# Kernel tuning notes

Hardware: AMD Instinct MI355X
Metric: run time of the kernel (lower is better)

Reference implementation:

```python
import jax, jax.numpy as jnp
import numpy as np

N_NODES = 100000
N_EDGES = 3200000
N_GRAPHS = 1000
HID = 64
L = 4  # num_unit


def setup_inputs() -> dict:
    key = jax.random.key(0)
    ks = jax.random.split(key, 16)
    x = jax.random.normal(ks[0], (N_NODES, 4), dtype=jnp.float32)
    edge_index = jax.random.randint(ks[1], (2, N_EDGES), 0, N_NODES, dtype=jnp.int64)
    edge_attr = jax.random.uniform(ks[2], (N_EDGES,), dtype=jnp.float32)
    batch = jnp.sort(jax.random.randint(ks[3], (N_NODES,), 0, N_GRAPHS, dtype=jnp.int64))
    s = 1.0 / np.sqrt(HID)
    inp = {
        'x': x, 'edge_index': edge_index, 'edge_attr': edge_attr, 'batch': batch,
        'emb_w': jax.random.normal(ks[4], (4, HID), jnp.float32) * 0.5,
        'emb_b': jnp.zeros((HID,), jnp.float32),
        'conv_w1': jax.random.normal(ks[5], (L, HID, HID), jnp.float32) * s,
        'conv_b1': jnp.zeros((L, HID), jnp.float32),
        'conv_w2': jax.random.normal(ks[6], (L, HID, HID), jnp.float32) * s,
        'conv_w3': jax.random.normal(ks[7], (L, HID, HID), jnp.float32) * s,
        'conv_b3': jnp.zeros((L, HID), jnp.float32),
        'lin1_w': jax.random.normal(ks[8], (HID, HID), jnp.float32) * s,
        'lin1_b': jnp.zeros((HID,), jnp.float32),
        'lin2_w': jax.random.normal(ks[9], (HID, 3), jnp.float32) * s,
        'lin2_b': jnp.zeros((3,), jnp.float32),
    }
    return inp


def _forward(x, edge_index, edge_attr, batch,
             emb_w, emb_b, conv_w1, conv_b1, conv_w2, conv_w3, conv_b3,
             lin1_w, lin1_b, lin2_w, lin2_b):
    src, dst = edge_index[0], edge_index[1]
    ew = edge_attr[:, None]  # [E,1]
    h = x @ emb_w + emb_b  # node_emb; dropout omitted (eval mode)
    for l in range(conv_w1.shape[0]):
        # LEConv: out_i = sum_{j->i} w_ji * (lin1(x_j) - lin2(x_i)) + lin3(x_i)
        a = h @ conv_w1[l] + conv_b1[l]
        b = h @ conv_w2[l]  # no bias
        msg = (a[src] - b[dst]) * ew  # [E, HID]
        agg = jax.ops.segment_sum(msg, dst, num_segments=h.shape[0])
        h = jax.nn.relu(agg + h @ conv_w3[l] + conv_b3[l])
    # global mean pool over graphs
    sums = jax.ops.segment_sum(h, batch, num_segments=N_GRAPHS)
    cnt = jax.ops.segment_sum(jnp.ones((h.shape[0],), h.dtype), batch, num_segments=N_GRAPHS)
    graph_x = sums / jnp.maximum(cnt, 1.0)[:, None]
    pred = jax.nn.relu(graph_x @ lin1_w + lin1_b) @ lin2_w + lin2_b
    return pred


def reference(x, edge_index, edge_attr, batch, emb_w, emb_b,
              conv_w1, conv_b1, conv_w2, conv_w3, conv_b3,
              lin1_w, lin1_b, lin2_w, lin2_b):
    return _forward(x, edge_index, edge_attr, batch, emb_w, emb_b,
                    conv_w1, conv_b1, conv_w2, conv_w3, conv_b3,
                    lin1_w, lin1_b, lin2_w, lin2_b)
```

## Files before the change

kernel.cpp:

```cpp
#include <hip/hip_runtime.h>

#define N_NODES 100000
#define N_EDGES 3200000
#define N_GRAPHS 1000
#define NLAYER 4
#define NB 391
#define CAP 8960
#define EPB 4096
#define NCHUNK 782

typedef __attribute__((ext_vector_type(8))) short bf16x8;
typedef __attribute__((ext_vector_type(4))) float f32x4;

static __device__ __forceinline__ unsigned f2bf(float f) {
  unsigned u = __float_as_uint(f);
  return (u + 0x7fffu + ((u >> 16) & 1u)) >> 16;
}
static __device__ __forceinline__ float bf2f_lo(unsigned u) {
  return __uint_as_float(u << 16);
}
static __device__ __forceinline__ float bf2f_hi(unsigned u) {
  return __uint_as_float(u & 0xffff0000u);
}

__global__ __launch_bounds__(256) void prologue_kernel(
    const float* __restrict__ x, const float* __restrict__ emb_w,
    const float* __restrict__ emb_b, unsigned short* __restrict__ h_bf,
    int* __restrict__ gcur,
    const float* __restrict__ cw1, const float* __restrict__ cw2,
    const float* __restrict__ cw3, unsigned* __restrict__ wswz)
{
  int tid = threadIdx.x;
  if (blockIdx.x == 4) {
    for (int i = tid; i < NB; i += 256) gcur[i] = i * CAP;
  }
  if (blockIdx.x < NLAYER) {
    int l = blockIdx.x;
    const float* w1 = cw1 + l * 4096;
    const float* w2 = cw2 + l * 4096;
    const float* w3 = cw3 + l * 4096;
    unsigned* outp = wswz + l * 6144;
    int n = tid & 63;
    int gofs = tid >> 6;
    for (int it = 0; it < 24; ++it) {
      int g = it * 4 + gofs;
      int m = g >> 5;
      int k = (g & 31) * 2;
      const float* W = (m == 0) ? w2 : (m == 1) ? w3 : w1;
      unsigned lo = f2bf(W[k * 64 + n]);
      unsigned hi = f2bf(W[(k + 1) * 64 + n]);
      int c = k >> 5;
      int kk = k & 31;
      int ln = ((kk >> 3) << 4) | (n & 15);
      int j2 = (kk & 7) >> 1;
      int t4 = n >> 4;
      outp[(((m * 2 + c) * 4 + t4) << 8) | (ln << 2) | j2] = lo | (hi << 16);
    }
  }
  int t = blockIdx.x * 256 + tid;
  if (t >= N_NODES * 64) return;
  int c = t & 63, v = t >> 6;
  float4 xv = ((const float4*)x)[v];
  float acc = emb_b[c];
  acc = fmaf(xv.x, emb_w[0 * 64 + c], acc);
  acc = fmaf(xv.y, emb_w[1 * 64 + c], acc);
  acc = fmaf(xv.z, emb_w[2 * 64 + c], acc);
  acc = fmaf(xv.w, emb_w[3 * 64 + c], acc);
  h_bf[t] = (unsigned short)f2bf(acc);
}

__global__ __launch_bounds__(256) void bscatter_kernel(
    const int* __restrict__ ei, const float* __restrict__ ea,
    int* __restrict__ gcur, unsigned* __restrict__ tmp_w,
    unsigned char* __restrict__ tmp_d)
{
  __shared__ unsigned hist[NB];
  __shared__ int dif[NB];
  __shared__ unsigned stage_w[EPB];
  __shared__ unsigned char stage_d[EPB];
  __shared__ unsigned short bid[EPB];
  __shared__ int wpart[4];
  int tid = threadIdx.x;
  int base = blockIdx.x * EPB;

  for (int i = tid; i < NB; i += 256) hist[i] = 0;
  __syncthreads();

  int dreg[16];
#pragma unroll
  for (int i = 0; i < 16; ++i) {
    int e = base + i * 256 + tid;
    dreg[i] = -1;
    if (e < N_EDGES) {
      int d = ei[N_EDGES + e];
      dreg[i] = d;
      atomicAdd(&hist[((unsigned)d) >> 8], 1u);
    }
  }
  __syncthreads();

  int lane = tid & 63, w = tid >> 6;
  int b0i = tid * 2, b1i = tid * 2 + 1;
  int c0 = (b0i < NB) ? (int)hist[b0i] : 0;
  int c1 = (b1i < NB) ? (int)hist[b1i] : 0;
  int tsum = c0 + c1;
  int s = tsum;
#pragma unroll
  for (int off = 1; off < 64; off <<= 1) {
    int y = __shfl_up(s, off);
    if (lane >= off) s += y;
  }
  if (lane == 63) wpart[w] = s;
  __syncthreads();
  int wo = 0;
  for (int ww = 0; ww < w; ++ww) wo += wpart[ww];
  int excl = wo + (s - tsum);
  if (b0i < NB) {
    int gb = c0 ? atomicAdd(&gcur[b0i], c0) : 0;
    dif[b0i] = gb - excl;
    hist[b0i] = (unsigned)excl;
  }
  if (b1i < NB) {
    int gb = c1 ? atomicAdd(&gcur[b1i], c1) : 0;
    dif[b1i] = gb - (excl + c0);
    hist[b1i] = (unsigned)(excl + c0);
  }
  __syncthreads();

#pragma unroll
  for (int i = 0; i < 16; ++i) {
    int e = base + i * 256 + tid;
    int d = dreg[i];
    if (d >= 0) {
      unsigned bkt = ((unsigned)d) >> 8;
      unsigned lp = atomicAdd(&hist[bkt], 1u);
      unsigned q15 = (unsigned)(ea[e] * 32768.0f);
      stage_w[lp] = ((unsigned)ei[e]) | (q15 << 17);
      stage_d[lp] = (unsigned char)(d & 255);
      bid[lp] = (unsigned short)bkt;
    }
  }
  __syncthreads();

  int nE = min(EPB, N_EDGES - base);
  for (int i = tid; i < nE; i += 256) {
    int g = dif[bid[i]] + i;
    tmp_w[g] = stage_w[i];
    tmp_d[g] = stage_d[i];
  }
}

__global__ __launch_bounds__(256) void bucket_sort_kernel(
    const int* __restrict__ gcur, const unsigned* __restrict__ tmp_w,
    const unsigned char* __restrict__ tmp_d,
    unsigned* __restrict__ csr, int* __restrict__ row_off,
    unsigned short* __restrict__ deg16, float* __restrict__ degw)
{
  int j = blockIdx.x;
  int b0 = j * CAP;
  int nE = min(gcur[j] - b0, CAP);
  __shared__ unsigned hist[256];
  __shared__ float dws[256];
  __shared__ unsigned cur[256];
  __shared__ int wpart[4];
  __shared__ unsigned short perm[CAP];
  int t = threadIdx.x;
  hist[t] = 0;
  dws[t] = 0.f;
  __syncthreads();
  for (int i = t; i < nE; i += 256) {
    unsigned d = tmp_d[b0 + i];
    unsigned wrd = tmp_w[b0 + i];
    atomicAdd(&hist[d], 1u);
    atomicAdd(&dws[d], (float)(wrd >> 17) * (1.0f / 32768.0f));
  }
  __syncthreads();
  int lane = t & 63, w = t >> 6;
  int v = (int)hist[t];
  int s = v;
#pragma unroll
  for (int off = 1; off < 64; off <<= 1) {
    int y = __shfl_up(s, off);
    if (lane >= off) s += y;
  }
  if (lane == 63) wpart[w] = s;
  __syncthreads();
  int wo = 0;
  for (int ww = 0; ww < w; ++ww) wo += wpart[ww];
  int excl = wo + s - v;
  cur[t] = (unsigned)excl;
  int vnode = (j << 8) + t;
  if (vnode < N_NODES) {
    row_off[vnode] = b0 + excl;
    deg16[vnode] = (unsigned short)v;
    degw[vnode] = dws[t];
  }
  __syncthreads();

  for (int i = t; i < nE; i += 256) {
    unsigned p = atomicAdd(&cur[tmp_d[b0 + i]], 1u);
    perm[p] = (unsigned short)i;
  }
  __syncthreads();
  for (int q = t; q < nE; q += 256)
    csr[b0 + q] = tmp_w[b0 + (int)perm[q]];
}

__global__ __launch_bounds__(256) void matvec3_mfma_kernel(
    const unsigned short* __restrict__ h_bf,
    const unsigned* __restrict__ wz,
    const float* __restrict__ b1, const float* __restrict__ b3,
    const float* __restrict__ degw,
    unsigned short* __restrict__ a_bf, unsigned short* __restrict__ cc_bf)
{
  int gw = (blockIdx.x * 256 + threadIdx.x) >> 6;
  int lane = threadIdx.x & 63;
  int quad = lane >> 4;
  int col = lane & 15;
  int nb = gw * 16;
  if (nb >= N_NODES) return;

  int arow = nb + col;
  if (arow >= N_NODES) arow = N_NODES - 1;
  const bf16x8* ap = (const bf16x8*)(h_bf + (size_t)arow * 64 + quad * 8);
  bf16x8 af0 = ap[0];
  bf16x8 af1 = ap[4];

  float dwr[4];
#pragma unroll
  for (int r = 0; r < 4; ++r) {
    int row = nb + quad * 4 + r;
    dwr[r] = degw[row < N_NODES ? row : 0];
  }

#pragma unroll
  for (int t = 0; t < 4; ++t) {
    const bf16x8* b20 = (const bf16x8*)&wz[((0 * 4 + t) << 8) + lane * 4];
    const bf16x8* b21 = (const bf16x8*)&wz[((1 * 4 + t) << 8) + lane * 4];
    const bf16x8* b30 = (const bf16x8*)&wz[((2 * 4 + t) << 8) + lane * 4];
    const bf16x8* b31 = (const bf16x8*)&wz[((3 * 4 + t) << 8) + lane * 4];
    const bf16x8* b10 = (const bf16x8*)&wz[((4 * 4 + t) << 8) + lane * 4];
    const bf16x8* b11 = (const bf16x8*)&wz[((5 * 4 + t) << 8) + lane * 4];

    f32x4 z = {0.f, 0.f, 0.f, 0.f};
    f32x4 acc2 = __builtin_amdgcn_mfma_f32_16x16x32_bf16(af0, *b20, z, 0, 0, 0);
    acc2 = __builtin_amdgcn_mfma_f32_16x16x32_bf16(af1, *b21, acc2, 0, 0, 0);
    f32x4 cc;
#pragma unroll
    for (int r = 0; r < 4; ++r) cc[r] = -dwr[r] * acc2[r];
    cc = __builtin_amdgcn_mfma_f32_16x16x32_bf16(af0, *b30, cc, 0, 0, 0);
    cc = __builtin_amdgcn_mfma_f32_16x16x32_bf16(af1, *b31, cc, 0, 0, 0);
    float bb3 = b3[t * 16 + col];
#pragma unroll
    for (int r = 0; r < 4; ++r) {
      int row = nb + quad * 4 + r;
      if (row < N_NODES)
        cc_bf[(size_t)row * 64 + t * 16 + col] = (unsigned short)f2bf(cc[r] + bb3);
    }

    float bb1 = b1[t * 16 + col];
    f32x4 a1 = {bb1, bb1, bb1, bb1};
    a1 = __builtin_amdgcn_mfma_f32_16x16x32_bf16(af0, *b10, a1, 0, 0, 0);
    a1 = __builtin_amdgcn_mfma_f32_16x16x32_bf16(af1, *b11, a1, 0, 0, 0);
#pragma unroll
    for (int r = 0; r < 4; ++r) {
      int row = nb + quad * 4 + r;
      if (row < N_NODES)
        a_bf[(size_t)row * 64 + t * 16 + col] = (unsigned short)f2bf(a1[r]);
    }
  }
}

__global__ __launch_bounds__(256) void agg_kernel(
    const uint2* __restrict__ a2, const uint2* __restrict__ cc2,
    const int* __restrict__ row_off, const unsigned short* __restrict__ deg16,
    const unsigned* __restrict__ csr,
    float4* __restrict__ h4, unsigned short* __restrict__ h_bf, int write_h)
{
  int wave = (blockIdx.x * 256 + threadIdx.x) >> 6;
  int lane = threadIdx.x & 63;
  int sg = lane >> 4;
  int li = lane & 15;
  int lsel = (lane & 48) << 2;
  int v = wave * 4 + sg;
  bool valid = v < N_NODES;
  int vc = valid ? v : N_NODES - 1;
  int base = row_off[vc];
  int ecnt = valid ? (int)deg16[vc] : 0;
  int emax = ecnt;
  emax = max(emax, __shfl_xor(emax, 16));
  emax = max(emax, __shfl_xor(emax, 32));

  float4 acc = make_float4(0.f, 0.f, 0.f, 0.f);
  if (valid) {
    uint2 cu = cc2[(size_t)vc * 16 + li];
    acc.x = bf2f_lo(cu.x);
    acc.y = bf2f_hi(cu.x);
    acc.z = bf2f_lo(cu.y);
    acc.w = bf2f_hi(cu.y);
  }
  const uint2* ap = a2 + li;

  int full = emax & ~15;
  int c0 = 0;
  for (; c0 < full; c0 += 16) {
    int idx = c0 + li;
    int er = (idx < ecnt) ? (int)csr[base + idx] : 0;
#pragma unroll
    for (int j = 0; j < 16; ++j) {
      unsigned r = (unsigned)__builtin_amdgcn_ds_bpermute(lsel | (j << 2), er);
      int s = (int)(r & 0x1FFFFu);
      float w = (float)(r >> 17) * (1.0f / 32768.0f);
      uint2 u = ap[(size_t)s * 16];
      acc.x = fmaf(w, bf2f_lo(u.x), acc.x);
      acc.y = fmaf(w, bf2f_hi(u.x), acc.y);
      acc.z = fmaf(w, bf2f_lo(u.y), acc.z);
      acc.w = fmaf(w, bf2f_hi(u.y), acc.w);
    }
  }
  int rem = emax - full;
  if (rem > 0) {
    int idx = c0 + li;
    int er = (idx < ecnt) ? (int)csr[base + idx] : 0;
    for (int j = 0; j < rem; ++j) {
      unsigned r = (unsigned)__builtin_amdgcn_ds_bpermute(lsel | (j << 2), er);
      int s = (int)(r & 0x1FFFFu);
      float w = (float)(r >> 17) * (1.0f / 32768.0f);
      uint2 u = ap[(size_t)s * 16];
      acc.x = fmaf(w, bf2f_lo(u.x), acc.x);
      acc.y = fmaf(w, bf2f_hi(u.x), acc.y);
      acc.z = fmaf(w, bf2f_lo(u.y), acc.z);
      acc.w = fmaf(w, bf2f_hi(u.y), acc.w);
    }
  }
  if (valid) {
    acc.x = fmaxf(acc.x, 0.f);
    acc.y = fmaxf(acc.y, 0.f);
    acc.z = fmaxf(acc.z, 0.f);
    acc.w = fmaxf(acc.w, 0.f);
    if (write_h) h4[(size_t)v * 16 + li] = acc;
    uint2 p;
    p.x = f2bf(acc.x) | (f2bf(acc.y) << 16);
    p.y = f2bf(acc.z) | (f2bf(acc.w) << 16);
    ((uint2*)h_bf)[(size_t)v * 16 + li] = p;
  }
}

__global__ __launch_bounds__(256) void head_kernel(
    const float* __restrict__ h, const int* __restrict__ batch,
    const float* __restrict__ l1w, const float* __restrict__ l1b,
    const float* __restrict__ l2w, const float* __restrict__ l2b,
    float* __restrict__ out)
{
  int g = (blockIdx.x * 256 + threadIdx.x) >> 6;
  int lane = threadIdx.x & 63;
  if (g >= N_GRAPHS) return;
  int lo = 0, hi = N_NODES;
  while (lo < hi) { int mid = (lo + hi) >> 1; if (batch[mid] < g) lo = mid + 1; else hi = mid; }
  int start = lo;
  hi = N_NODES;
  while (lo < hi) { int mid = (lo + hi) >> 1; if (batch[mid] < g + 1) lo = mid + 1; else hi = mid; }
  int end = lo;

  float sum = 0.f;
  for (int v = start; v < end; ++v) sum += h[(size_t)v * 64 + lane];
  float cntf = (float)(end - start);
  float gx = sum / fmaxf(cntf, 1.f);

  float acc = l1b[lane];
  for (int k = 0; k < 64; ++k) {
    float gxk = __shfl(gx, k);
    acc = fmaf(gxk, l1w[k * 64 + lane], acc);
  }
  float t = fmaxf(acc, 0.f);
  float p0 = t * l2w[lane * 3 + 0];
  float p1 = t * l2w[lane * 3 + 1];
  float p2 = t * l2w[lane * 3 + 2];
  for (int off = 32; off > 0; off >>= 1) {
    p0 += __shfl_down(p0, off);
    p1 += __shfl_down(p1, off);
    p2 += __shfl_down(p2, off);
  }
  if (lane == 0) {
    out[g * 3 + 0] = p0 + l2b[0];
    out[g * 3 + 1] = p1 + l2b[1];
    out[g * 3 + 2] = p2 + l2b[2];
  }
}

extern "C" void kernel_launch(void* const* d_in, const int* in_sizes, int n_in,
                              void* d_out, int out_size, void* d_ws, size_t ws_size,
                              hipStream_t stream)
{
  (void)in_sizes; (void)n_in; (void)out_size; (void)ws_size;
  const float* x     = (const float*)d_in[0];
  const int*   ei    = (const int*)d_in[1];
  const float* ea    = (const float*)d_in[2];
  const int*   batch = (const int*)d_in[3];
  const float* emb_w = (const float*)d_in[4];
  const float* emb_b = (const float*)d_in[5];
  const float* cw1   = (const float*)d_in[6];
  const float* cb1   = (const float*)d_in[7];
  const float* cw2   = (const float*)d_in[8];
  const float* cw3   = (const float*)d_in[9];
  const float* cb3   = (const float*)d_in[10];
  const float* l1w   = (const float*)d_in[11];
  const float* l1b   = (const float*)d_in[12];
  const float* l2w   = (const float*)d_in[13];
  const float* l2b   = (const float*)d_in[14];
  float* out = (float*)d_out;

  char* wsb = (char*)d_ws;
  size_t off = 0;
  auto alloc = [&](size_t bytes) {
    char* p = wsb + off;
    off = (off + bytes + 255) & ~(size_t)255;
    return p;
  };
  float* h       = (float*)alloc(sizeof(float) * (size_t)N_NODES * 64);
  unsigned short* h_bf = (unsigned short*)alloc(sizeof(short) * (size_t)N_NODES * 64);
  unsigned short* a_bf = (unsigned short*)alloc(sizeof(short) * (size_t)N_NODES * 64);
  unsigned short* cc_bf = (unsigned short*)alloc(sizeof(short) * (size_t)N_NODES * 64);
  unsigned* csr  = (unsigned*)alloc(sizeof(unsigned) * (size_t)NB * CAP);
  int*   row_off = (int*)alloc(sizeof(int) * N_NODES);
  unsigned short* deg16 = (unsigned short*)alloc(sizeof(short) * N_NODES);
  float* degw    = (float*)alloc(sizeof(float) * N_NODES);
  int*   gcur    = (int*)alloc(sizeof(int) * NB);
  unsigned* wswz = (unsigned*)alloc(sizeof(unsigned) * NLAYER * 6144);
  unsigned* tmp_w = (unsigned*)h;
  unsigned char* tmp_d = (unsigned char*)h + sizeof(unsigned) * (size_t)NB * CAP;

  prologue_kernel<<<(N_NODES * 64 + 255) / 256, 256, 0, stream>>>(
      x, emb_w, emb_b, h_bf, gcur, cw1, cw2, cw3, wswz);
  bscatter_kernel<<<NCHUNK, 256, 0, stream>>>(ei, ea, gcur, tmp_w, tmp_d);
  bucket_sort_kernel<<<NB, 256, 0, stream>>>(gcur, tmp_w, tmp_d, csr, row_off,
                                             deg16, degw);

  int agg_blocks = (N_NODES + 15) / 16;
  int mv_blocks = (N_NODES / 16 + 3) / 4 + 1;
  for (int l = 0; l < NLAYER; ++l) {
    matvec3_mfma_kernel<<<mv_blocks, 256, 0, stream>>>(
        h_bf, wswz + l * 6144, cb1 + l * 64, cb3 + l * 64, degw, a_bf, cc_bf);
    agg_kernel<<<agg_blocks, 256, 0, stream>>>(
        (const uint2*)a_bf, (const uint2*)cc_bf, row_off, deg16, csr, (float4*)h,
        h_bf, (l == NLAYER - 1) ? 1 : 0);
  }

  head_kernel<<<(N_GRAPHS * 64 + 255) / 256, 256, 0, stream>>>(
      h, batch, l1w, l1b, l2w, l2b, out);
}
```

Before: 520.2 us.

## Fuse per-layer matvec, aggregation and head into one persistent kernel with grid barriers

Replaces the eight per-layer launches plus the head launch with a single persistent kernel sized by occupancy. A hierarchical software grid barrier separates the matvec and aggregation phases, and the tiles and node groups are walked with grid-stride loops. The bucket scatter now loads edge source and weight in the first pass and keeps them in registers. This removes launch gaps and tail effects between small kernels. In exchange the kernel risks barrier overhead, lower occupancy from the 8-blocks-per-CU bound, and deadlock if not all blocks are co-resident.

```diff
diff --git a/kernel.cpp b/kernel.cpp
--- a/kernel.cpp
+++ b/kernel.cpp
@@ -8,6 +8,10 @@
 #define CAP 8960
 #define EPB 4096
 #define NCHUNK 782
+#define N_TILES 6250
+#define N_GRP 25000
+#define MAXBLK 2048
+#define BAR_LINES 66
 
 typedef __attribute__((ext_vector_type(8))) short bf16x8;
 typedef __attribute__((ext_vector_type(4))) float f32x4;
@@ -21,6 +25,34 @@
 }
 static __device__ __forceinline__ float bf2f_hi(unsigned u) {
   return __uint_as_float(u & 0xffff0000u);
+}
+
+static __device__ __forceinline__ void gbar(int* bar, int bid, int nblk) {
+  __syncthreads();
+  if (threadIdx.x == 0) {
+    __threadfence();
+    int gen = __hip_atomic_load(bar + 65 * 32, __ATOMIC_RELAXED,
+                                __HIP_MEMORY_SCOPE_AGENT);
+    int* leaf = bar + (bid >> 5) * 32;
+    int old = __hip_atomic_fetch_add(leaf, 1, __ATOMIC_RELAXED,
+                                     __HIP_MEMORY_SCOPE_AGENT);
+    if (old == 31) {
+      __hip_atomic_store(leaf, 0, __ATOMIC_RELAXED, __HIP_MEMORY_SCOPE_AGENT);
+      int rold = __hip_atomic_fetch_add(bar + 64 * 32, 1, __ATOMIC_RELAXED,
+                                        __HIP_MEMORY_SCOPE_AGENT);
+      if (rold == (nblk >> 5) - 1) {
+        __hip_atomic_store(bar + 64 * 32, 0, __ATOMIC_RELAXED,
+                           __HIP_MEMORY_SCOPE_AGENT);
+        __hip_atomic_fetch_add(bar + 65 * 32, 1, __ATOMIC_RELAXED,
+                               __HIP_MEMORY_SCOPE_AGENT);
+      }
+    }
+    while (__hip_atomic_load(bar + 65 * 32, __ATOMIC_RELAXED,
+                             __HIP_MEMORY_SCOPE_AGENT) == gen)
+      __builtin_amdgcn_s_sleep(16);
+    __threadfence();
+  }
+  __syncthreads();
 }
 
 __global__ __launch_bounds__(256) void prologue_kernel(
@@ -28,11 +60,15 @@
     const float* __restrict__ emb_b, unsigned short* __restrict__ h_bf,
     int* __restrict__ gcur,
     const float* __restrict__ cw1, const float* __restrict__ cw2,
-    const float* __restrict__ cw3, unsigned* __restrict__ wswz)
+    const float* __restrict__ cw3, unsigned* __restrict__ wswz,
+    int* __restrict__ bar)
 {
   int tid = threadIdx.x;
   if (blockIdx.x == 4) {
     for (int i = tid; i < NB; i += 256) gcur[i] = i * CAP;
+  }
+  if (blockIdx.x == 5) {
+    for (int i = tid; i < BAR_LINES * 32; i += 256) bar[i] = 0;
   }
   if (blockIdx.x < NLAYER) {
     int l = blockIdx.x;
@@ -87,6 +123,7 @@
   __syncthreads();
 
   int dreg[16];
+  unsigned wreg[16];
 #pragma unroll
   for (int i = 0; i < 16; ++i) {
     int e = base + i * 256 + tid;
@@ -94,6 +131,8 @@
     if (e < N_EDGES) {
       int d = ei[N_EDGES + e];
       dreg[i] = d;
+      unsigned q15 = (unsigned)(ea[e] * 32768.0f);
+      wreg[i] = ((unsigned)ei[e]) | (q15 << 17);
       atomicAdd(&hist[((unsigned)d) >> 8], 1u);
     }
   }
@@ -129,13 +168,11 @@
 
 #pragma unroll
   for (int i = 0; i < 16; ++i) {
-    int e = base + i * 256 + tid;
     int d = dreg[i];
     if (d >= 0) {
       unsigned bkt = ((unsigned)d) >> 8;
       unsigned lp = atomicAdd(&hist[bkt], 1u);
-      unsigned q15 = (unsigned)(ea[e] * 32768.0f);
-      stage_w[lp] = ((unsigned)ei[e]) | (q15 << 17);
+      stage_w[lp] = wreg[i];
       stage_d[lp] = (unsigned char)(d & 255);
       bid[lp] = (unsigned short)bkt;
     }
@@ -206,185 +243,175 @@
     csr[b0 + q] = tmp_w[b0 + (int)perm[q]];
 }
 
-__global__ __launch_bounds__(256) void matvec3_mfma_kernel(
-    const unsigned short* __restrict__ h_bf,
-    const unsigned* __restrict__ wz,
-    const float* __restrict__ b1, const float* __restrict__ b3,
-    const float* __restrict__ degw,
-    unsigned short* __restrict__ a_bf, unsigned short* __restrict__ cc_bf)
+__global__ __launch_bounds__(256, 8) void layers_kernel(
+    unsigned short* __restrict__ h_bf, unsigned short* __restrict__ a_bf,
+    unsigned short* __restrict__ cc_bf, const unsigned* __restrict__ csr,
+    const int* __restrict__ row_off, const unsigned short* __restrict__ deg16,
+    const float* __restrict__ degw, const unsigned* __restrict__ wswz,
+    const float* __restrict__ cb1, const float* __restrict__ cb3,
+    float* __restrict__ h, const int* __restrict__ batch,
+    const float* __restrict__ l1w, const float* __restrict__ l1b,
+    const float* __restrict__ l2w, const float* __restrict__ l2b,
+    float* __restrict__ out, int* __restrict__ bar, int nblk)
 {
-  int gw = (blockIdx.x * 256 + threadIdx.x) >> 6;
-  int lane = threadIdx.x & 63;
+  int bid = blockIdx.x;
+  int tid = threadIdx.x;
+  int lane = tid & 63;
+  int gw = bid * 4 + (tid >> 6);
+  int nwave = nblk * 4;
   int quad = lane >> 4;
   int col = lane & 15;
-  int nb = gw * 16;
-  if (nb >= N_NODES) return;
-
-  int arow = nb + col;
-  if (arow >= N_NODES) arow = N_NODES - 1;
-  const bf16x8* ap = (const bf16x8*)(h_bf + (size_t)arow * 64 + quad * 8);
-  bf16x8 af0 = ap[0];
-  bf16x8 af1 = ap[4];
-
-  float dwr[4];
-#pragma unroll
-  for (int r = 0; r < 4; ++r) {
-    int row = nb + quad * 4 + r;
-    dwr[r] = degw[row < N_NODES ? row : 0];
-  }
-
-#pragma unroll
-  for (int t = 0; t < 4; ++t) {
-    const bf16x8* b20 = (const bf16x8*)&wz[((0 * 4 + t) << 8) + lane * 4];
-    const bf16x8* b21 = (const bf16x8*)&wz[((1 * 4 + t) << 8) + lane * 4];
-    const bf16x8* b30 = (const bf16x8*)&wz[((2 * 4 + t) << 8) + lane * 4];
-    const bf16x8* b31 = (const bf16x8*)&wz[((3 * 4 + t) << 8) + lane * 4];
-    const bf16x8* b10 = (const bf16x8*)&wz[((4 * 4 + t) << 8) + lane * 4];
-    const bf16x8* b11 = (const bf16x8*)&wz[((5 * 4 + t) << 8) + lane * 4];
-
-    f32x4 z = {0.f, 0.f, 0.f, 0.f};
-    f32x4 acc2 = __builtin_amdgcn_mfma_f32_16x16x32_bf16(af0, *b20, z, 0, 0, 0);
-    acc2 = __builtin_amdgcn_mfma_f32_16x16x32_bf16(af1, *b21, acc2, 0, 0, 0);
-    f32x4 cc;
-#pragma unroll
-    for (int r = 0; r < 4; ++r) cc[r] = -dwr[r] * acc2[r];
-    cc = __builtin_amdgcn_mfma_f32_16x16x32_bf16(af0, *b30, cc, 0, 0, 0);
-    cc = __builtin_amdgcn_mfma_f32_16x16x32_bf16(af1, *b31, cc, 0, 0, 0);
-    float bb3 = b3[t * 16 + col];
-#pragma unroll
-    for (int r = 0; r < 4; ++r) {
-      int row = nb + quad * 4 + r;
-      if (row < N_NODES)
-        cc_bf[(size_t)row * 64 + t * 16 + col] = (unsigned short)f2bf(cc[r] + bb3);
-    }
-
-    float bb1 = b1[t * 16 + col];
-    f32x4 a1 = {bb1, bb1, bb1, bb1};
-    a1 = __builtin_amdgcn_mfma_f32_16x16x32_bf16(af0, *b10, a1, 0, 0, 0);
-    a1 = __builtin_amdgcn_mfma_f32_16x16x32_bf16(af1, *b11, a1, 0, 0, 0);
-#pragma unroll
-    for (int r = 0; r < 4; ++r) {
-      int row = nb + quad * 4 + r;
-      if (row < N_NODES)
-        a_bf[(size_t)row * 64 + t * 16 + col] = (unsigned short)f2bf(a1[r]);
-    }
-  }
-}
-
-__global__ __launch_bounds__(256) void agg_kernel(
-    const uint2* __restrict__ a2, const uint2* __restrict__ cc2,
-    const int* __restrict__ row_off, const unsigned short* __restrict__ deg16,
-    const unsigned* __restrict__ csr,
-    float4* __restrict__ h4, unsigned short* __restrict__ h_bf, int write_h)
-{
-  int wave = (blockIdx.x * 256 + threadIdx.x) >> 6;
-  int lane = threadIdx.x & 63;
   int sg = lane >> 4;
   int li = lane & 15;
   int lsel = (lane & 48) << 2;
-  int v = wave * 4 + sg;
-  bool valid = v < N_NODES;
-  int vc = valid ? v : N_NODES - 1;
-  int base = row_off[vc];
-  int ecnt = valid ? (int)deg16[vc] : 0;
-  int emax = ecnt;
-  emax = max(emax, __shfl_xor(emax, 16));
-  emax = max(emax, __shfl_xor(emax, 32));
-
-  float4 acc = make_float4(0.f, 0.f, 0.f, 0.f);
-  if (valid) {
-    uint2 cu = cc2[(size_t)vc * 16 + li];
-    acc.x = bf2f_lo(cu.x);
-    acc.y = bf2f_hi(cu.x);
-    acc.z = bf2f_lo(cu.y);
-    acc.w = bf2f_hi(cu.y);
-  }
-  const uint2* ap = a2 + li;
-
-  int full = emax & ~15;
-  int c0 = 0;
-  for (; c0 < full; c0 += 16) {
-    int idx = c0 + li;
-    int er = (idx < ecnt) ? (int)csr[base + idx] : 0;
-#pragma unroll
-    for (int j = 0; j < 16; ++j) {
-      unsigned r = (unsigned)__builtin_amdgcn_ds_bpermute(lsel | (j << 2), er);
-      int s = (int)(r & 0x1FFFFu);
-      float w = (float)(r >> 17) * (1.0f / 32768.0f);
-      uint2 u = ap[(size_t)s * 16];
-      acc.x = fmaf(w, bf2f_lo(u.x), acc.x);
-      acc.y = fmaf(w, bf2f_hi(u.x), acc.y);
-      acc.z = fmaf(w, bf2f_lo(u.y), acc.z);
-      acc.w = fmaf(w, bf2f_hi(u.y), acc.w);
-    }
-  }
-  int rem = emax - full;
-  if (rem > 0) {
-    int idx = c0 + li;
-    int er = (idx < ecnt) ? (int)csr[base + idx] : 0;
-    for (int j = 0; j < rem; ++j) {
-      unsigned r = (unsigned)__builtin_amdgcn_ds_bpermute(lsel | (j << 2), er);
-      int s = (int)(r & 0x1FFFFu);
-      float w = (float)(r >> 17) * (1.0f / 32768.0f);
-      uint2 u = ap[(size_t)s * 16];
-      acc.x = fmaf(w, bf2f_lo(u.x), acc.x);
-      acc.y = fmaf(w, bf2f_hi(u.x), acc.y);
-      acc.z = fmaf(w, bf2f_lo(u.y), acc.z);
-      acc.w = fmaf(w, bf2f_hi(u.y), acc.w);
-    }
-  }
-  if (valid) {
-    acc.x = fmaxf(acc.x, 0.f);
-    acc.y = fmaxf(acc.y, 0.f);
-    acc.z = fmaxf(acc.z, 0.f);
-    acc.w = fmaxf(acc.w, 0.f);
-    if (write_h) h4[(size_t)v * 16 + li] = acc;
-    uint2 p;
-    p.x = f2bf(acc.x) | (f2bf(acc.y) << 16);
-    p.y = f2bf(acc.z) | (f2bf(acc.w) << 16);
-    ((uint2*)h_bf)[(size_t)v * 16 + li] = p;
-  }
-}
-
-__global__ __launch_bounds__(256) void head_kernel(
-    const float* __restrict__ h, const int* __restrict__ batch,
-    const float* __restrict__ l1w, const float* __restrict__ l1b,
-    const float* __restrict__ l2w, const float* __restrict__ l2b,
-    float* __restrict__ out)
-{
-  int g = (blockIdx.x * 256 + threadIdx.x) >> 6;
-  int lane = threadIdx.x & 63;
-  if (g >= N_GRAPHS) return;
-  int lo = 0, hi = N_NODES;
-  while (lo < hi) { int mid = (lo + hi) >> 1; if (batch[mid] < g) lo = mid + 1; else hi = mid; }
-  int start = lo;
-  hi = N_NODES;
-  while (lo < hi) { int mid = (lo + hi) >> 1; if (batch[mid] < g + 1) lo = mid + 1; else hi = mid; }
-  int end = lo;
-
-  float sum = 0.f;
-  for (int v = start; v < end; ++v) sum += h[(size_t)v * 64 + lane];
-  float cntf = (float)(end - start);
-  float gx = sum / fmaxf(cntf, 1.f);
-
-  float acc = l1b[lane];
-  for (int k = 0; k < 64; ++k) {
-    float gxk = __shfl(gx, k);
-    acc = fmaf(gxk, l1w[k * 64 + lane], acc);
-  }
-  float t = fmaxf(acc, 0.f);
-  float p0 = t * l2w[lane * 3 + 0];
-  float p1 = t * l2w[lane * 3 + 1];
-  float p2 = t * l2w[lane * 3 + 2];
-  for (int off = 32; off > 0; off >>= 1) {
-    p0 += __shfl_down(p0, off);
-    p1 += __shfl_down(p1, off);
-    p2 += __shfl_down(p2, off);
-  }
-  if (lane == 0) {
-    out[g * 3 + 0] = p0 + l2b[0];
-    out[g * 3 + 1] = p1 + l2b[1];
-    out[g * 3 + 2] = p2 + l2b[2];
+
+  for (int l = 0; l < NLAYER; ++l) {
+    const unsigned* wz = wswz + l * 6144;
+    const float* b1 = cb1 + l * 64;
+    const float* b3 = cb3 + l * 64;
+
+    for (int tile = gw; tile < N_TILES; tile += nwave) {
+      int nb = tile * 16;
+      int arow = nb + col;
+      const bf16x8* ap = (const bf16x8*)(h_bf + (size_t)arow * 64 + quad * 8);
+      bf16x8 af0 = ap[0];
+      bf16x8 af1 = ap[4];
+      float dwr[4];
+#pragma unroll
+      for (int r = 0; r < 4; ++r) dwr[r] = degw[nb + quad * 4 + r];
+
+#pragma unroll
+      for (int t = 0; t < 4; ++t) {
+        const bf16x8* b20 = (const bf16x8*)&wz[((0 * 4 + t) << 8) + lane * 4];
+        const bf16x8* b21 = (const bf16x8*)&wz[((1 * 4 + t) << 8) + lane * 4];
+        const bf16x8* b30 = (const bf16x8*)&wz[((2 * 4 + t) << 8) + lane * 4];
+        const bf16x8* b31 = (const bf16x8*)&wz[((3 * 4 + t) << 8) + lane * 4];
+        const bf16x8* b10 = (const bf16x8*)&wz[((4 * 4 + t) << 8) + lane * 4];
+        const bf16x8* b11 = (const bf16x8*)&wz[((5 * 4 + t) << 8) + lane * 4];
+
+        f32x4 z = {0.f, 0.f, 0.f, 0.f};
+        f32x4 acc2 = __builtin_amdgcn_mfma_f32_16x16x32_bf16(af0, *b20, z, 0, 0, 0);
+        acc2 = __builtin_amdgcn_mfma_f32_16x16x32_bf16(af1, *b21, acc2, 0, 0, 0);
+        f32x4 cc;
+#pragma unroll
+        for (int r = 0; r < 4; ++r) cc[r] = -dwr[r] * acc2[r];
+        cc = __builtin_amdgcn_mfma_f32_16x16x32_bf16(af0, *b30, cc, 0, 0, 0);
+        cc = __builtin_amdgcn_mfma_f32_16x16x32_bf16(af1, *b31, cc, 0, 0, 0);
+        float bb3 = b3[t * 16 + col];
+#pragma unroll
+        for (int r = 0; r < 4; ++r) {
+          int row = nb + quad * 4 + r;
+          cc_bf[(size_t)row * 64 + t * 16 + col] = (unsigned short)f2bf(cc[r] + bb3);
+        }
+        float bb1 = b1[t * 16 + col];
+        f32x4 a1 = {bb1, bb1, bb1, bb1};
+        a1 = __builtin_amdgcn_mfma_f32_16x16x32_bf16(af0, *b10, a1, 0, 0, 0);
+        a1 = __builtin_amdgcn_mfma_f32_16x16x32_bf16(af1, *b11, a1, 0, 0, 0);
+#pragma unroll
+        for (int r = 0; r < 4; ++r) {
+          int row = nb + quad * 4 + r;
+          a_bf[(size_t)row * 64 + t * 16 + col] = (unsigned short)f2bf(a1[r]);
+        }
+      }
+    }
+    gbar(bar, bid, nblk);
+
+    const uint2* a2 = (const uint2*)a_bf;
+    const uint2* cc2 = (const uint2*)cc_bf;
+    int write_h = (l == NLAYER - 1);
+    for (int grp = gw; grp < N_GRP; grp += nwave) {
+      int v = grp * 4 + sg;
+      int base = row_off[v];
+      int ecnt = (int)deg16[v];
+      int emax = ecnt;
+      emax = max(emax, __shfl_xor(emax, 16));
+      emax = max(emax, __shfl_xor(emax, 32));
+
+      uint2 cu = cc2[(size_t)v * 16 + li];
+      float4 acc;
+      acc.x = bf2f_lo(cu.x);
+      acc.y = bf2f_hi(cu.x);
+      acc.z = bf2f_lo(cu.y);
+      acc.w = bf2f_hi(cu.y);
+      const uint2* ap = a2 + li;
+
+      int full = emax & ~15;
+      int c0 = 0;
+      for (; c0 < full; c0 += 16) {
+        int idx = c0 + li;
+        int er = (idx < ecnt) ? (int)csr[base + idx] : 0;
+#pragma unroll
+        for (int j = 0; j < 16; ++j) {
+          unsigned r = (unsigned)__builtin_amdgcn_ds_bpermute(lsel | (j << 2), er);
+          int s = (int)(r & 0x1FFFFu);
+          float w = (float)(r >> 17) * (1.0f / 32768.0f);
+          uint2 u = ap[(size_t)s * 16];
+          acc.x = fmaf(w, bf2f_lo(u.x), acc.x);
+          acc.y = fmaf(w, bf2f_hi(u.x), acc.y);
+          acc.z = fmaf(w, bf2f_lo(u.y), acc.z);
+          acc.w = fmaf(w, bf2f_hi(u.y), acc.w);
+        }
+      }
+      int rem = emax - full;
+      if (rem > 0) {
+        int idx = c0 + li;
+        int er = (idx < ecnt) ? (int)csr[base + idx] : 0;
+        for (int j = 0; j < rem; ++j) {
+          unsigned r = (unsigned)__builtin_amdgcn_ds_bpermute(lsel | (j << 2), er);
+          int s = (int)(r & 0x1FFFFu);
+          float w = (float)(r >> 17) * (1.0f / 32768.0f);
+          uint2 u = ap[(size_t)s * 16];
+          acc.x = fmaf(w, bf2f_lo(u.x), acc.x);
+          acc.y = fmaf(w, bf2f_hi(u.x), acc.y);
+          acc.z = fmaf(w, bf2f_lo(u.y), acc.z);
+          acc.w = fmaf(w, bf2f_hi(u.y), acc.w);
+        }
+      }
+      acc.x = fmaxf(acc.x, 0.f);
+      acc.y = fmaxf(acc.y, 0.f);
+      acc.z = fmaxf(acc.z, 0.f);
+      acc.w = fmaxf(acc.w, 0.f);
+      if (write_h) ((float4*)h)[(size_t)v * 16 + li] = acc;
+      uint2 p;
+      p.x = f2bf(acc.x) | (f2bf(acc.y) << 16);
+      p.y = f2bf(acc.z) | (f2bf(acc.w) << 16);
+      ((uint2*)h_bf)[(size_t)v * 16 + li] = p;
+    }
+    gbar(bar, bid, nblk);
+  }
+
+  for (int g = gw; g < N_GRAPHS; g += nwave) {
+    int lo = 0, hi = N_NODES;
+    while (lo < hi) { int mid = (lo + hi) >> 1; if (batch[mid] < g) lo = mid + 1; else hi = mid; }
+    int start = lo;
+    hi = N_NODES;
+    while (lo < hi) { int mid = (lo + hi) >> 1; if (batch[mid] < g + 1) lo = mid + 1; else hi = mid; }
+    int end = lo;
+
+    float sum = 0.f;
+    for (int v = start; v < end; ++v) sum += h[(size_t)v * 64 + lane];
+    float cntf = (float)(end - start);
+    float gx = sum / fmaxf(cntf, 1.f);
+
+    float acc = l1b[lane];
+    for (int k = 0; k < 64; ++k) {
+      float gxk = __shfl(gx, k);
+      acc = fmaf(gxk, l1w[k * 64 + lane], acc);
+    }
+    float t = fmaxf(acc, 0.f);
+    float p0 = t * l2w[lane * 3 + 0];
+    float p1 = t * l2w[lane * 3 + 1];
+    float p2 = t * l2w[lane * 3 + 2];
+    for (int off = 32; off > 0; off >>= 1) {
+      p0 += __shfl_down(p0, off);
+      p1 += __shfl_down(p1, off);
+      p2 += __shfl_down(p2, off);
+    }
+    if (lane == 0) {
+      out[g * 3 + 0] = p0 + l2b[0];
+      out[g * 3 + 1] = p1 + l2b[1];
+      out[g * 3 + 2] = p2 + l2b[2];
+    }
   }
 }
 
@@ -427,25 +454,24 @@
   float* degw    = (float*)alloc(sizeof(float) * N_NODES);
   int*   gcur    = (int*)alloc(sizeof(int) * NB);
   unsigned* wswz = (unsigned*)alloc(sizeof(unsigned) * NLAYER * 6144);
+  int*   bar     = (int*)alloc(sizeof(int) * BAR_LINES * 32);
   unsigned* tmp_w = (unsigned*)h;
   unsigned char* tmp_d = (unsigned char*)h + sizeof(unsigned) * (size_t)NB * CAP;
 
+  int maxb = 0;
+  hipOccupancyMaxActiveBlocksPerMultiprocessor(&maxb, layers_kernel, 256, 0);
+  if (maxb < 1) maxb = 1;
+  int nblk = maxb * 256;
+  if (nblk > MAXBLK) nblk = MAXBLK;
+  nblk = (nblk / 32) * 32;
+  if (nblk < 32) nblk = 32;
+
   prologue_kernel<<<(N_NODES * 64 + 255) / 256, 256, 0, stream>>>(
-      x, emb_w, emb_b, h_bf, gcur, cw1, cw2, cw3, wswz);
+      x, emb_w, emb_b, h_bf, gcur, cw1, cw2, cw3, wswz, bar);
   bscatter_kernel<<<NCHUNK, 256, 0, stream>>>(ei, ea, gcur, tmp_w, tmp_d);
   bucket_sort_kernel<<<NB, 256, 0, stream>>>(gcur, tmp_w, tmp_d, csr, row_off,
                                              deg16, degw);
-
-  int agg_blocks = (N_NODES + 15) / 16;
-  int mv_blocks = (N_NODES / 16 + 3) / 4 + 1;
-  for (int l = 0; l < NLAYER; ++l) {
-    matvec3_mfma_kernel<<<mv_blocks, 256, 0, stream>>>(
-        h_bf, wswz + l * 6144, cb1 + l * 64, cb3 + l * 64, degw, a_bf, cc_bf);
-    agg_kernel<<<agg_blocks, 256, 0, stream>>>(
-        (const uint2*)a_bf, (const uint2*)cc_bf, row_off, deg16, csr, (float4*)h,
-        h_bf, (l == NLAYER - 1) ? 1 : 0);
-  }
-
-  head_kernel<<<(N_GRAPHS * 64 + 255) / 256, 256, 0, stream>>>(
-      h, batch, l1w, l1b, l2w, l2b, out);
-}
+  layers_kernel<<<nblk, 256, 0, stream>>>(
+      h_bf, a_bf, cc_bf, csr, row_off, deg16, degw, wswz, cb1, cb3,
+      h, batch, l1w, l1b, l2w, l2b, out, bar, nblk);
+}
```

Measured after the change: 1.100 ms. 2.11x slower.

## Fuse next-layer MFMA matvec into aggregation kernel with ping-pong buffers

Applied to the files above, without the earlier changes.

Each aggregation block now handles 64 nodes, stages their bf16 outputs in shared memory, and computes the next layer's a/cc projections with MFMA before writing them out. The node features no longer make a global round trip through h_bf, and three kernel launches are removed, using double-buffered a/cc arrays. Separately, the bucket scatter loads source index and edge weight in the first pass and keeps them in registers instead of re-reading them. The fused kernel needs a block barrier and extra LDS, which may reduce occupancy for the latency-bound gather.

```diff
diff --git a/kernel.cpp b/kernel.cpp
--- a/kernel.cpp
+++ b/kernel.cpp
@@ -8,6 +8,7 @@
 #define CAP 8960
 #define EPB 4096
 #define NCHUNK 782
+#define NFBLK 1563
 
 typedef __attribute__((ext_vector_type(8))) short bf16x8;
 typedef __attribute__((ext_vector_type(4))) float f32x4;
@@ -87,6 +88,7 @@
   __syncthreads();
 
   int dreg[16];
+  unsigned wreg[16];
 #pragma unroll
   for (int i = 0; i < 16; ++i) {
     int e = base + i * 256 + tid;
@@ -94,6 +96,8 @@
     if (e < N_EDGES) {
       int d = ei[N_EDGES + e];
       dreg[i] = d;
+      unsigned q15 = (unsigned)(ea[e] * 32768.0f);
+      wreg[i] = ((unsigned)ei[e]) | (q15 << 17);
       atomicAdd(&hist[((unsigned)d) >> 8], 1u);
     }
   }
@@ -129,13 +133,11 @@
 
 #pragma unroll
   for (int i = 0; i < 16; ++i) {
-    int e = base + i * 256 + tid;
     int d = dreg[i];
     if (d >= 0) {
       unsigned bkt = ((unsigned)d) >> 8;
       unsigned lp = atomicAdd(&hist[bkt], 1u);
-      unsigned q15 = (unsigned)(ea[e] * 32768.0f);
-      stage_w[lp] = ((unsigned)ei[e]) | (q15 << 17);
+      stage_w[lp] = wreg[i];
       stage_d[lp] = (unsigned char)(d & 255);
       bid[lp] = (unsigned short)bkt;
     }
@@ -206,7 +208,7 @@
     csr[b0 + q] = tmp_w[b0 + (int)perm[q]];
 }
 
-__global__ __launch_bounds__(256) void matvec3_mfma_kernel(
+__global__ __launch_bounds__(256) void matvec0_kernel(
     const unsigned short* __restrict__ h_bf,
     const unsigned* __restrict__ wz,
     const float* __restrict__ b1, const float* __restrict__ b3,
@@ -271,78 +273,142 @@
   }
 }
 
-__global__ __launch_bounds__(256) void agg_kernel(
+__global__ __launch_bounds__(256) void aggmv_kernel(
     const uint2* __restrict__ a2, const uint2* __restrict__ cc2,
     const int* __restrict__ row_off, const unsigned short* __restrict__ deg16,
-    const unsigned* __restrict__ csr,
-    float4* __restrict__ h4, unsigned short* __restrict__ h_bf, int write_h)
-{
-  int wave = (blockIdx.x * 256 + threadIdx.x) >> 6;
-  int lane = threadIdx.x & 63;
+    const unsigned* __restrict__ csr, const float* __restrict__ degw,
+    const unsigned* __restrict__ wz,
+    const float* __restrict__ b1, const float* __restrict__ b3,
+    unsigned short* __restrict__ a_out, unsigned short* __restrict__ cc_out,
+    float4* __restrict__ h4, int write_h, int do_mv)
+{
+  __shared__ uint2 hl[64][18];
+  int tid = threadIdx.x;
+  int lane = tid & 63;
+  int wv = tid >> 6;
   int sg = lane >> 4;
   int li = lane & 15;
   int lsel = (lane & 48) << 2;
-  int v = wave * 4 + sg;
-  bool valid = v < N_NODES;
-  int vc = valid ? v : N_NODES - 1;
-  int base = row_off[vc];
-  int ecnt = valid ? (int)deg16[vc] : 0;
-  int emax = ecnt;
-  emax = max(emax, __shfl_xor(emax, 16));
-  emax = max(emax, __shfl_xor(emax, 32));
-
-  float4 acc = make_float4(0.f, 0.f, 0.f, 0.f);
-  if (valid) {
-    uint2 cu = cc2[(size_t)vc * 16 + li];
-    acc.x = bf2f_lo(cu.x);
-    acc.y = bf2f_hi(cu.x);
-    acc.z = bf2f_lo(cu.y);
-    acc.w = bf2f_hi(cu.y);
-  }
-  const uint2* ap = a2 + li;
-
-  int full = emax & ~15;
-  int c0 = 0;
-  for (; c0 < full; c0 += 16) {
-    int idx = c0 + li;
-    int er = (idx < ecnt) ? (int)csr[base + idx] : 0;
-#pragma unroll
-    for (int j = 0; j < 16; ++j) {
-      unsigned r = (unsigned)__builtin_amdgcn_ds_bpermute(lsel | (j << 2), er);
-      int s = (int)(r & 0x1FFFFu);
-      float w = (float)(r >> 17) * (1.0f / 32768.0f);
-      uint2 u = ap[(size_t)s * 16];
-      acc.x = fmaf(w, bf2f_lo(u.x), acc.x);
-      acc.y = fmaf(w, bf2f_hi(u.x), acc.y);
-      acc.z = fmaf(w, bf2f_lo(u.y), acc.z);
-      acc.w = fmaf(w, bf2f_hi(u.y), acc.w);
-    }
-  }
-  int rem = emax - full;
-  if (rem > 0) {
-    int idx = c0 + li;
-    int er = (idx < ecnt) ? (int)csr[base + idx] : 0;
-    for (int j = 0; j < rem; ++j) {
-      unsigned r = (unsigned)__builtin_amdgcn_ds_bpermute(lsel | (j << 2), er);
-      int s = (int)(r & 0x1FFFFu);
-      float w = (float)(r >> 17) * (1.0f / 32768.0f);
-      uint2 u = ap[(size_t)s * 16];
-      acc.x = fmaf(w, bf2f_lo(u.x), acc.x);
-      acc.y = fmaf(w, bf2f_hi(u.x), acc.y);
-      acc.z = fmaf(w, bf2f_lo(u.y), acc.z);
-      acc.w = fmaf(w, bf2f_hi(u.y), acc.w);
-    }
-  }
-  if (valid) {
-    acc.x = fmaxf(acc.x, 0.f);
-    acc.y = fmaxf(acc.y, 0.f);
-    acc.z = fmaxf(acc.z, 0.f);
-    acc.w = fmaxf(acc.w, 0.f);
-    if (write_h) h4[(size_t)v * 16 + li] = acc;
-    uint2 p;
-    p.x = f2bf(acc.x) | (f2bf(acc.y) << 16);
-    p.y = f2bf(acc.z) | (f2bf(acc.w) << 16);
-    ((uint2*)h_bf)[(size_t)v * 16 + li] = p;
+  int nb0 = blockIdx.x * 64;
+
+#pragma unroll
+  for (int it = 0; it < 4; ++it) {
+    int lv = wv * 16 + it * 4 + sg;
+    int v = nb0 + lv;
+    bool valid = v < N_NODES;
+    int vc = valid ? v : N_NODES - 1;
+    int base = row_off[vc];
+    int ecnt = valid ? (int)deg16[vc] : 0;
+    int emax = ecnt;
+    emax = max(emax, __shfl_xor(emax, 16));
+    emax = max(emax, __shfl_xor(emax, 32));
+
+    float4 acc = make_float4(0.f, 0.f, 0.f, 0.f);
+    if (valid) {
+      uint2 cu = cc2[(size_t)vc * 16 + li];
+      acc.x = bf2f_lo(cu.x);
+      acc.y = bf2f_hi(cu.x);
+      acc.z = bf2f_lo(cu.y);
+      acc.w = bf2f_hi(cu.y);
+    }
+    const uint2* ap = a2 + li;
+
+    int full = emax & ~15;
+    int c0 = 0;
+    for (; c0 < full; c0 += 16) {
+      int idx = c0 + li;
+      int er = (idx < ecnt) ? (int)csr[base + idx] : 0;
+#pragma unroll
+      for (int j = 0; j < 16; ++j) {
+        unsigned r = (unsigned)__builtin_amdgcn_ds_bpermute(lsel | (j << 2), er);
+        int s = (int)(r & 0x1FFFFu);
+        float w = (float)(r >> 17) * (1.0f / 32768.0f);
+        uint2 u = ap[(size_t)s * 16];
+        acc.x = fmaf(w, bf2f_lo(u.x), acc.x);
+        acc.y = fmaf(w, bf2f_hi(u.x), acc.y);
+        acc.z = fmaf(w, bf2f_lo(u.y), acc.z);
+        acc.w = fmaf(w, bf2f_hi(u.y), acc.w);
+      }
+    }
+    int rem = emax - full;
+    if (rem > 0) {
+      int idx = c0 + li;
+      int er = (idx < ecnt) ? (int)csr[base + idx] : 0;
+      for (int j = 0; j < rem; ++j) {
+        unsigned r = (unsigned)__builtin_amdgcn_ds_bpermute(lsel | (j << 2), er);
+        int s = (int)(r & 0x1FFFFu);
+        float w = (float)(r >> 17) * (1.0f / 32768.0f);
+        uint2 u = ap[(size_t)s * 16];
+        acc.x = fmaf(w, bf2f_lo(u.x), acc.x);
+        acc.y = fmaf(w, bf2f_hi(u.x), acc.y);
+        acc.z = fmaf(w, bf2f_lo(u.y), acc.z);
+        acc.w = fmaf(w, bf2f_hi(u.y), acc.w);
+      }
+    }
+    if (valid) {
+      acc.x = fmaxf(acc.x, 0.f);
+      acc.y = fmaxf(acc.y, 0.f);
+      acc.z = fmaxf(acc.z, 0.f);
+      acc.w = fmaxf(acc.w, 0.f);
+      if (write_h) h4[(size_t)v * 16 + li] = acc;
+      uint2 p;
+      p.x = f2bf(acc.x) | (f2bf(acc.y) << 16);
+      p.y = f2bf(acc.z) | (f2bf(acc.w) << 16);
+      hl[lv][li] = p;
+    }
+  }
+  if (!do_mv) return;
+  __syncthreads();
+
+  int quad = lane >> 4;
+  int col = lane & 15;
+  int nb = nb0 + wv * 16;
+  const char* rowp = (const char*)&hl[wv * 16 + col][0];
+  bf16x8 af0 = *(const bf16x8*)(rowp + quad * 16);
+  bf16x8 af1 = *(const bf16x8*)(rowp + 64 + quad * 16);
+
+  float dwr[4];
+#pragma unroll
+  for (int r = 0; r < 4; ++r) {
+    int row = nb + quad * 4 + r;
+    dwr[r] = degw[row < N_NODES ? row : 0];
+  }
+
+#pragma unroll
+  for (int t = 0; t < 4; ++t) {
+    const bf16x8* b20 = (const bf16x8*)&wz[((0 * 4 + t) << 8) + lane * 4];
+    const bf16x8* b21 = (const bf16x8*)&wz[((1 * 4 + t) << 8) + lane * 4];
+    const bf16x8* b30 = (const bf16x8*)&wz[((2 * 4 + t) << 8) + lane * 4];
+    const bf16x8* b31 = (const bf16x8*)&wz[((3 * 4 + t) << 8) + lane * 4];
+    const bf16x8* b10 = (const bf16x8*)&wz[((4 * 4 + t) << 8) + lane * 4];
+    const bf16x8* b11 = (const bf16x8*)&wz[((5 * 4 + t) << 8) + lane * 4];
+
+    f32x4 z = {0.f, 0.f, 0.f, 0.f};
+    f32x4 acc2 = __builtin_amdgcn_mfma_f32_16x16x32_bf16(af0, *b20, z, 0, 0, 0);
+    acc2 = __builtin_amdgcn_mfma_f32_16x16x32_bf16(af1, *b21, acc2, 0, 0, 0);
+    f32x4 cc;
+#pragma unroll
+    for (int r = 0; r < 4; ++r) cc[r] = -dwr[r] * acc2[r];
+    cc = __builtin_amdgcn_mfma_f32_16x16x32_bf16(af0, *b30, cc, 0, 0, 0);
+    cc = __builtin_amdgcn_mfma_f32_16x16x32_bf16(af1, *b31, cc, 0, 0, 0);
+    float bb3 = b3[t * 16 + col];
+#pragma unroll
+    for (int r = 0; r < 4; ++r) {
+      int row = nb + quad * 4 + r;
+      if (row < N_NODES)
+        cc_out[(size_t)row * 64 + t * 16 + col] = (unsigned short)f2bf(cc[r] + bb3);
+    }
+
+    float bb1 = b1[t * 16 + col];
+    f32x4 a1 = {bb1, bb1, bb1, bb1};
+    a1 = __builtin_amdgcn_mfma_f32_16x16x32_bf16(af0, *b10, a1, 0, 0, 0);
+    a1 = __builtin_amdgcn_mfma_f32_16x16x32_bf16(af1, *b11, a1, 0, 0, 0);
+#pragma unroll
+    for (int r = 0; r < 4; ++r) {
+      int row = nb + quad * 4 + r;
+      if (row < N_NODES)
+        a_out[(size_t)row * 64 + t * 16 + col] = (unsigned short)f2bf(a1[r]);
+    }
   }
 }
 
@@ -419,8 +485,10 @@
   };
   float* h       = (float*)alloc(sizeof(float) * (size_t)N_NODES * 64);
   unsigned short* h_bf = (unsigned short*)alloc(sizeof(short) * (size_t)N_NODES * 64);
-  unsigned short* a_bf = (unsigned short*)alloc(sizeof(short) * (size_t)N_NODES * 64);
-  unsigned short* cc_bf = (unsigned short*)alloc(sizeof(short) * (size_t)N_NODES * 64);
+  unsigned short* a0   = (unsigned short*)alloc(sizeof(short) * (size_t)N_NODES * 64);
+  unsigned short* cc0  = (unsigned short*)alloc(sizeof(short) * (size_t)N_NODES * 64);
+  unsigned short* a1   = (unsigned short*)alloc(sizeof(short) * (size_t)N_NODES * 64);
+  unsigned short* cc1  = (unsigned short*)alloc(sizeof(short) * (size_t)N_NODES * 64);
   unsigned* csr  = (unsigned*)alloc(sizeof(unsigned) * (size_t)NB * CAP);
   int*   row_off = (int*)alloc(sizeof(int) * N_NODES);
   unsigned short* deg16 = (unsigned short*)alloc(sizeof(short) * N_NODES);
@@ -436,14 +504,21 @@
   bucket_sort_kernel<<<NB, 256, 0, stream>>>(gcur, tmp_w, tmp_d, csr, row_off,
                                              deg16, degw);
 
-  int agg_blocks = (N_NODES + 15) / 16;
   int mv_blocks = (N_NODES / 16 + 3) / 4 + 1;
+  matvec0_kernel<<<mv_blocks, 256, 0, stream>>>(
+      h_bf, wswz, cb1, cb3, degw, a0, cc0);
+
+  unsigned short* ain = a0;  unsigned short* ccin = cc0;
+  unsigned short* aout = a1; unsigned short* ccout = cc1;
   for (int l = 0; l < NLAYER; ++l) {
-    matvec3_mfma_kernel<<<mv_blocks, 256, 0, stream>>>(
-        h_bf, wswz + l * 6144, cb1 + l * 64, cb3 + l * 64, degw, a_bf, cc_bf);
-    agg_kernel<<<agg_blocks, 256, 0, stream>>>(
-        (const uint2*)a_bf, (const uint2*)cc_bf, row_off, deg16, csr, (float4*)h,
-        h_bf, (l == NLAYER - 1) ? 1 : 0);
+    int last = (l == NLAYER - 1);
+    aggmv_kernel<<<NFBLK, 256, 0, stream>>>(
+        (const uint2*)ain, (const uint2*)ccin, row_off, deg16, csr, degw,
+        wswz + (last ? 0 : (l + 1) * 6144),
+        cb1 + (last ? 0 : (l + 1) * 64), cb3 + (last ? 0 : (l + 1) * 64),
+        aout, ccout, (float4*)h, last ? 1 : 0, last ? 0 : 1);
+    unsigned short* ta = ain; ain = aout; aout = ta;
+    unsigned short* tc = ccin; ccin = ccout; ccout = tc;
   }
 
   head_kernel<<<(N_GRAPHS * 64 + 255) / 256, 256, 0, stream>>>(
```

Result: slower. 552.0 us (+6.1%).
